# Optimization experiments

Hardware: AMD Instinct MI355X
Metric: run time of the kernel (lower is better)

Reference implementation:

```python
import jax, jax.numpy as jnp
import numpy as np
import math

T, B, N, D = 4, 4, 1024, 512
H = 8
HD = D // H
EPS = 1e-6


def setup_inputs() -> dict:
    key = jax.random.key(0)
    ks = jax.random.split(key, 9)
    s = 1.0 / math.sqrt(D)
    inp = {"x": jax.random.normal(ks[0], (T, B, N, D), dtype=jnp.float32)}
    names = ["wq", "wk", "wv", "wo"]
    for i, nm in enumerate(names):
        inp[nm] = jax.random.uniform(ks[1 + i], (D, D), dtype=jnp.float32, minval=-s, maxval=s)
        inp["b" + nm[1]] = jax.random.uniform(ks[5 + i], (D,), dtype=jnp.float32, minval=-s, maxval=s)
    return inp


def reference(x, wq, bq, wk, bk, wv, bv, wo, bo):
    t, b, n, d = x.shape
    # torch Linear: y = x @ W.T + bias
    q = x @ wq.T + bq
    k = x @ wk.T + bk
    v = x @ wv.T + bv
    # (t, b, n, H, HD) -> (t, b, H, n, HD)
    qh = q.reshape(t, b, n, H, HD).transpose(0, 1, 3, 2, 4)
    kh = k.reshape(t, b, n, H, HD).transpose(0, 1, 3, 2, 4)
    vh = v.reshape(t, b, n, H, HD).transpose(0, 1, 3, 2, 4)
    scores = jnp.einsum("tbhqd,tbhkd->tbhqk", qh, kh) / math.sqrt(HD)
    attn = jax.nn.relu(scores)
    attn = attn / (attn.sum(axis=-1, keepdims=True) + EPS)
    ctx = jnp.einsum("tbhqk,tbhkd->tbhqd", attn, vh)
    out = ctx.transpose(0, 1, 3, 2, 4).reshape(t, b, n, d)
    return out @ wo.T + bo
```

## Files before the change

### kernel.cpp

```cpp
#include <hip/hip_runtime.h>

typedef unsigned short u16;
typedef __attribute__((ext_vector_type(8))) short bf16x8;
typedef __attribute__((ext_vector_type(4))) float f32x4;
typedef __attribute__((ext_vector_type(16))) float f32x16;
typedef __attribute__((ext_vector_type(2))) unsigned int u32x2;

__device__ inline u16 f2b(float f) {
    unsigned u;
    __builtin_memcpy(&u, &f, 4);
    unsigned r = u + 0x7FFF + ((u >> 16) & 1);
    return (u16)(r >> 16);
}

__device__ inline bf16x8 pack8(const float* p) {
    union { u16 us[8]; bf16x8 v; } r;
#pragma unroll
    for (int i = 0; i < 8; i++) r.us[i] = f2b(p[i]);
    return r.v;
}

__device__ inline unsigned cvtpk(float lo, float hi) {
    unsigned r;
    asm("v_cvt_pk_bf16_f32 %0, %1, %2" : "=v"(r) : "v"(lo), "v"(hi));
    return r;
}

__device__ inline void gload16(const void* g, void* l) {
    __builtin_amdgcn_global_load_lds((__attribute__((address_space(1))) void*)g,
                                     (__attribute__((address_space(3))) void*)l, 16, 0, 0);
}

__global__ __launch_bounds__(256) void conv_kernel(const float* __restrict__ x,
                                                   const float* __restrict__ wq,
                                                   const float* __restrict__ wk,
                                                   const float* __restrict__ wv,
                                                   const float* __restrict__ wo,
                                                   u16* __restrict__ xb, u16* __restrict__ wb) {
    const int bid = blockIdx.x;
    const float* src;
    u16* dst;
    size_t base;
    if (bid < 4096) {
        src = x; dst = xb; base = (size_t)bid * 2048;
    } else {
        const int wsel = (bid - 4096) >> 7;
        src = (wsel == 0) ? wq : (wsel == 1) ? wk : (wsel == 2) ? wv : wo;
        dst = wb + (size_t)wsel * 262144;
        base = (size_t)((bid - 4096) & 127) * 2048;
    }
    const size_t idx = base + (size_t)threadIdx.x * 8;
    float a[8];
    *(float4*)&a[0] = *(const float4*)&src[idx];
    *(float4*)&a[4] = *(const float4*)&src[idx + 4];
    *(bf16x8*)&dst[idx] = pack8(a);
}

template <int MODE>
__global__ __launch_bounds__(256) void gemm_kernel(const u16* __restrict__ A,
                                                   const u16* __restrict__ W,
                                                   const float* __restrict__ B0,
                                                   const float* __restrict__ B1,
                                                   const float* __restrict__ B2,
                                                   void* __restrict__ O0v, u16* __restrict__ O1,
                                                   u16* __restrict__ O2) {
    const int m0 = blockIdx.x * 128;
    const int n0 = blockIdx.y * 128;
    const int seg = (MODE == 0) ? (n0 >> 9) : 0;
    const int nl0 = (MODE == 0) ? (n0 & 511) : n0;
    const float* Bb = (seg == 0) ? B0 : (seg == 1) ? B1 : B2;
    u16* O = (seg == 0) ? (u16*)O0v : (seg == 1) ? O1 : O2;

    __shared__ __align__(16) u16 Al[128 * 32];
    __shared__ __align__(16) u16 Bl[128 * 32];

    const int tid = threadIdx.x;
    const int lane = tid & 63, wave = tid >> 6;
    const int quad = lane >> 4, col = lane & 15;
    const int wm = wave >> 1, wn = wave & 1;

    f32x4 acc[4][4];
#pragma unroll
    for (int i = 0; i < 4; i++)
#pragma unroll
        for (int j = 0; j < 4; j++) acc[i][j] = (f32x4){0.f, 0.f, 0.f, 0.f};

    for (int k0 = 0; k0 < 512; k0 += 32) {
#pragma unroll
        for (int sh = 0; sh < 4; sh++) {
            const int c = tid + sh * 256;
            const int cl = c & 511;
            const int row = cl >> 2, cc = (cl & 3) * 8;
            if (c < 512)
                gload16(&A[(size_t)(m0 + row) * 512 + k0 + cc], &Al[cl * 8]);
            else
                gload16(&W[(size_t)(n0 + row) * 512 + k0 + cc], &Bl[cl * 8]);
        }
        __syncthreads();
        bf16x8 af[4], bfr[4];
#pragma unroll
        for (int t = 0; t < 4; t++) {
            af[t] = *(const bf16x8*)&Al[(wm * 64 + t * 16 + col) * 32 + quad * 8];
            bfr[t] = *(const bf16x8*)&Bl[(wn * 64 + t * 16 + col) * 32 + quad * 8];
        }
#pragma unroll
        for (int i = 0; i < 4; i++)
#pragma unroll
            for (int j = 0; j < 4; j++)
                acc[i][j] = __builtin_amdgcn_mfma_f32_16x16x32_bf16(af[i], bfr[j], acc[i][j], 0, 0, 0);
        __syncthreads();
    }

    float bias[4];
#pragma unroll
    for (int j = 0; j < 4; j++) bias[j] = Bb[nl0 + wn * 64 + j * 16 + col];

#pragma unroll
    for (int i = 0; i < 4; i++) {
        const int mbase = m0 + wm * 64 + i * 16 + quad * 4;
#pragma unroll
        for (int j = 0; j < 4; j++) {
            const int nl = nl0 + wn * 64 + j * 16 + col;
            if (MODE == 1) {
                float* Of = (float*)O0v;
#pragma unroll
                for (int r = 0; r < 4; r++)
                    Of[(size_t)(mbase + r) * 512 + nl] = acc[i][j][r] + bias[j];
            } else {
                const int h = nl >> 6, hd = nl & 63;
                if (seg < 2) {
                    const float qs = (seg == 0) ? 0.125f : 1.f;
#pragma unroll
                    for (int r = 0; r < 4; r++) {
                        int m = mbase + r;
                        int s = m >> 10, tok = m & 1023;
                        O[(size_t)((s * 8 + h) * 1024 + tok) * 64 + hd] =
                            f2b((acc[i][j][r] + bias[j]) * qs);
                    }
                } else {
                    int s = mbase >> 10, tok0 = mbase & 1023;
                    union { u16 us[4]; uint2 v; } pk;
#pragma unroll
                    for (int r = 0; r < 4; r++) pk.us[r] = f2b(acc[i][j][r] + bias[j]);
                    *(uint2*)&O[(size_t)((s * 8 + h) * 64 + hd) * 1024 + tok0] = pk.v;
                }
            }
        }
    }
}

__global__ __launch_bounds__(256) void attn_kernel(const u16* __restrict__ Q,
                                                   const u16* __restrict__ Kp,
                                                   const u16* __restrict__ Vt,
                                                   u16* __restrict__ Ctx) {
    __shared__ __align__(16) u16 Kl[2][4096];
    __shared__ __align__(16) u16 Vl[2][4096];

    const int bid = blockIdx.x;
    const int head = bid & 127;
    const int qt = bid >> 7;
    const int s = head >> 3, h = head & 7;
    const u16* Qh = Q + (size_t)head * 65536;
    const u16* Kh = Kp + (size_t)head * 65536;
    const u16* Vh = Vt + (size_t)head * 65536;

    const int tid = threadIdx.x;
    const int lane = tid & 63, wave = tid >> 6;
    const int l31 = lane & 31, hi = lane >> 5;
    const int q0 = qt * 128 + wave * 32;
    const int cx = l31 & 7;

    int srow[2], sxc[2];
#pragma unroll
    for (int i = 0; i < 2; i++) {
        const int p = tid + i * 256;
        srow[i] = p >> 3;
        sxc[i] = (p & 7) ^ (srow[i] & 7);
    }

#define STAGE(B, K0)                                                                  \
    {                                                                                 \
        _Pragma("unroll") for (int i_ = 0; i_ < 2; i_++) {                            \
            const int p_ = tid + i_ * 256;                                            \
            gload16(&Kh[(size_t)((K0) + srow[i_]) * 64 + sxc[i_] * 8], &Kl[B][p_ * 8]); \
        }                                                                             \
        _Pragma("unroll") for (int i_ = 0; i_ < 2; i_++) {                            \
            const int p_ = tid + i_ * 256;                                            \
            gload16(&Vh[(size_t)srow[i_] * 1024 + (K0) + sxc[i_] * 8], &Vl[B][p_ * 8]); \
        }                                                                             \
    }

    union { u16 us[8]; bf16x8 v; } one;
#pragma unroll
    for (int i = 0; i < 8; i++) one.us[i] = 0x3F80;
    const bf16x8 onesf = one.v;

    bf16x8 qf[4];
#pragma unroll
    for (int kk = 0; kk < 4; kk++)
        qf[kk] = *(const bf16x8*)&Qh[(size_t)(q0 + l31) * 64 + kk * 16 + hi * 8];

    f32x16 cacc[2], dacc;
#pragma unroll
    for (int r = 0; r < 16; r++) { cacc[0][r] = 0.f; cacc[1][r] = 0.f; dacc[r] = 0.f; }

    STAGE(0, 0)
    __syncthreads();

    int buf = 0;
    for (int kt = 0; kt < 16; kt++) {
        if (kt < 15) STAGE(buf ^ 1, (kt + 1) * 64)

        bf16x8 pa[4];
#pragma unroll
        for (int mt = 0; mt < 2; mt++) {
            f32x16 sacc;
#pragma unroll
            for (int r = 0; r < 16; r++) sacc[r] = 0.f;
            __builtin_amdgcn_s_setprio(1);
#pragma unroll
            for (int kk = 0; kk < 4; kk++) {
                const bf16x8 kf =
                    *(const bf16x8*)&Kl[buf][((mt * 32 + l31) * 8 + ((2 * kk + hi) ^ cx)) * 8];
                sacc = __builtin_amdgcn_mfma_f32_32x32x16_bf16(kf, qf[kk], sacc, 0, 0, 0);
            }
            __builtin_amdgcn_s_setprio(0);

            const unsigned c0 = cvtpk(fmaxf(sacc[0], 0.f), fmaxf(sacc[1], 0.f));
            const unsigned c1 = cvtpk(fmaxf(sacc[2], 0.f), fmaxf(sacc[3], 0.f));
            const unsigned c2 = cvtpk(fmaxf(sacc[4], 0.f), fmaxf(sacc[5], 0.f));
            const unsigned c3 = cvtpk(fmaxf(sacc[6], 0.f), fmaxf(sacc[7], 0.f));
            const unsigned c4 = cvtpk(fmaxf(sacc[8], 0.f), fmaxf(sacc[9], 0.f));
            const unsigned c5 = cvtpk(fmaxf(sacc[10], 0.f), fmaxf(sacc[11], 0.f));
            const unsigned c6 = cvtpk(fmaxf(sacc[12], 0.f), fmaxf(sacc[13], 0.f));
            const unsigned c7 = cvtpk(fmaxf(sacc[14], 0.f), fmaxf(sacc[15], 0.f));
            const u32x2 s02 = __builtin_amdgcn_permlane32_swap(c0, c2, false, false);
            const u32x2 s13 = __builtin_amdgcn_permlane32_swap(c1, c3, false, false);
            const u32x2 s46 = __builtin_amdgcn_permlane32_swap(c4, c6, false, false);
            const u32x2 s57 = __builtin_amdgcn_permlane32_swap(c5, c7, false, false);
            union { unsigned u[4]; bf16x8 v; } f0, f1;
            f0.u[0] = s02.x; f0.u[1] = s13.x; f0.u[2] = s02.y; f0.u[3] = s13.y;
            f1.u[0] = s46.x; f1.u[1] = s57.x; f1.u[2] = s46.y; f1.u[3] = s57.y;
            pa[mt * 2 + 0] = f0.v;
            pa[mt * 2 + 1] = f1.v;
        }

        __builtin_amdgcn_s_setprio(1);
#pragma unroll
        for (int kg = 0; kg < 4; kg++) {
            const bf16x8 vf0 = *(const bf16x8*)&Vl[buf][(l31 * 8 + ((2 * kg + hi) ^ cx)) * 8];
            const bf16x8 vf1 =
                *(const bf16x8*)&Vl[buf][(((32 + l31)) * 8 + ((2 * kg + hi) ^ cx)) * 8];
            dacc = __builtin_amdgcn_mfma_f32_32x32x16_bf16(pa[kg], onesf, dacc, 0, 0, 0);
            cacc[0] = __builtin_amdgcn_mfma_f32_32x32x16_bf16(pa[kg], vf0, cacc[0], 0, 0, 0);
            cacc[1] = __builtin_amdgcn_mfma_f32_32x32x16_bf16(pa[kg], vf1, cacc[1], 0, 0, 0);
        }
        __builtin_amdgcn_s_setprio(0);

        __syncthreads();
        buf ^= 1;
    }
#undef STAGE

#pragma unroll
    for (int r = 0; r < 16; r++) {
        const int ql = (r & 3) + 8 * (r >> 2) + 4 * hi;
        const float inv = 1.f / (dacc[r] + 1e-6f);
        const size_t grow = (size_t)(s * 1024 + q0 + ql);
        Ctx[grow * 512 + h * 64 + l31] = f2b(cacc[0][r] * inv);
        Ctx[grow * 512 + h * 64 + 32 + l31] = f2b(cacc[1][r] * inv);
    }
}

extern "C" void kernel_launch(void* const* d_in, const int* in_sizes, int n_in, void* d_out,
                              int out_size, void* d_ws, size_t ws_size, hipStream_t stream) {
    const float* x = (const float*)d_in[0];
    const float* wq = (const float*)d_in[1];
    const float* bq = (const float*)d_in[2];
    const float* wk = (const float*)d_in[3];
    const float* bk = (const float*)d_in[4];
    const float* wv = (const float*)d_in[5];
    const float* bv = (const float*)d_in[6];
    const float* wo = (const float*)d_in[7];
    const float* bo = (const float*)d_in[8];

    const size_t E = 16384ull * 512ull;
    u16* xb = (u16*)d_ws;
    u16* cw = xb;
    u16* wb = xb + E;
    u16* qw = wb + 4 * 262144;
    u16* kw = qw + E;
    u16* vw = kw + E;

    conv_kernel<<<dim3(4096 + 512), 256, 0, stream>>>(x, wq, wk, wv, wo, xb, wb);
    gemm_kernel<0><<<dim3(128, 12), 256, 0, stream>>>(xb, wb, bq, bk, bv, qw, kw, vw);
    attn_kernel<<<dim3(1024), 256, 0, stream>>>(qw, kw, vw, cw);
    gemm_kernel<1><<<dim3(128, 4), 256, 0, stream>>>(cw, wb + 3 * 262144, bo, nullptr, nullptr,
                                                     d_out, nullptr, nullptr);
}
```

Measured before the change: 206.7 us.

## Double attention query tile per wave to reuse staged K/V fragments

Each wave now handles 64 query rows instead of 32, so a block covers 256 queries and the grid is halved to 512 blocks. Every K and V fragment read from shared memory feeds two MFMA chains, which halves K/V global staging and LDS reads per query. A launch-bounds hint of 2 blocks per CU is added. The cost is twice the accumulator registers per wave, which may lower occupancy, and fewer blocks to spread across the CUs.

```diff
diff --git a/kernel.cpp b/kernel.cpp
--- a/kernel.cpp
+++ b/kernel.cpp
@@ -149,10 +149,10 @@
     }
 }
 
-__global__ __launch_bounds__(256) void attn_kernel(const u16* __restrict__ Q,
-                                                   const u16* __restrict__ Kp,
-                                                   const u16* __restrict__ Vt,
-                                                   u16* __restrict__ Ctx) {
+__global__ __launch_bounds__(256, 2) void attn_kernel(const u16* __restrict__ Q,
+                                                      const u16* __restrict__ Kp,
+                                                      const u16* __restrict__ Vt,
+                                                      u16* __restrict__ Ctx) {
     __shared__ __align__(16) u16 Kl[2][4096];
     __shared__ __align__(16) u16 Vl[2][4096];
 
@@ -167,7 +167,7 @@
     const int tid = threadIdx.x;
     const int lane = tid & 63, wave = tid >> 6;
     const int l31 = lane & 31, hi = lane >> 5;
-    const int q0 = qt * 128 + wave * 32;
+    const int q0 = qt * 256 + wave * 64;
     const int cx = l31 & 7;
 
     int srow[2], sxc[2];
@@ -178,16 +178,16 @@
         sxc[i] = (p & 7) ^ (srow[i] & 7);
     }
 
-#define STAGE(B, K0)                                                                  \
-    {                                                                                 \
-        _Pragma("unroll") for (int i_ = 0; i_ < 2; i_++) {                            \
-            const int p_ = tid + i_ * 256;                                            \
+#define STAGE(B, K0)                                                                    \
+    {                                                                                   \
+        _Pragma("unroll") for (int i_ = 0; i_ < 2; i_++) {                              \
+            const int p_ = tid + i_ * 256;                                              \
             gload16(&Kh[(size_t)((K0) + srow[i_]) * 64 + sxc[i_] * 8], &Kl[B][p_ * 8]); \
-        }                                                                             \
-        _Pragma("unroll") for (int i_ = 0; i_ < 2; i_++) {                            \
-            const int p_ = tid + i_ * 256;                                            \
+        }                                                                               \
+        _Pragma("unroll") for (int i_ = 0; i_ < 2; i_++) {                              \
+            const int p_ = tid + i_ * 256;                                              \
             gload16(&Vh[(size_t)srow[i_] * 1024 + (K0) + sxc[i_] * 8], &Vl[B][p_ * 8]); \
-        }                                                                             \
+        }                                                                               \
     }
 
     union { u16 us[8]; bf16x8 v; } one;
@@ -195,14 +195,25 @@
     for (int i = 0; i < 8; i++) one.us[i] = 0x3F80;
     const bf16x8 onesf = one.v;
 
-    bf16x8 qf[4];
-#pragma unroll
-    for (int kk = 0; kk < 4; kk++)
-        qf[kk] = *(const bf16x8*)&Qh[(size_t)(q0 + l31) * 64 + kk * 16 + hi * 8];
-
-    f32x16 cacc[2], dacc;
-#pragma unroll
-    for (int r = 0; r < 16; r++) { cacc[0][r] = 0.f; cacc[1][r] = 0.f; dacc[r] = 0.f; }
+    bf16x8 qf[2][4];
+#pragma unroll
+    for (int q2 = 0; q2 < 2; q2++)
+#pragma unroll
+        for (int kk = 0; kk < 4; kk++)
+            qf[q2][kk] =
+                *(const bf16x8*)&Qh[(size_t)(q0 + q2 * 32 + l31) * 64 + kk * 16 + hi * 8];
+
+    f32x16 cacc[2][2];
+    f32x16 dacc[2];
+#pragma unroll
+    for (int q2 = 0; q2 < 2; q2++) {
+#pragma unroll
+        for (int r = 0; r < 16; r++) {
+            cacc[q2][0][r] = 0.f;
+            cacc[q2][1][r] = 0.f;
+            dacc[q2][r] = 0.f;
+        }
+    }
 
     STAGE(0, 0)
     __syncthreads();
@@ -211,38 +222,43 @@
     for (int kt = 0; kt < 16; kt++) {
         if (kt < 15) STAGE(buf ^ 1, (kt + 1) * 64)
 
-        bf16x8 pa[4];
+        bf16x8 pa[2][4];
 #pragma unroll
         for (int mt = 0; mt < 2; mt++) {
-            f32x16 sacc;
-#pragma unroll
-            for (int r = 0; r < 16; r++) sacc[r] = 0.f;
+            f32x16 s0, s1;
+#pragma unroll
+            for (int r = 0; r < 16; r++) { s0[r] = 0.f; s1[r] = 0.f; }
             __builtin_amdgcn_s_setprio(1);
 #pragma unroll
             for (int kk = 0; kk < 4; kk++) {
                 const bf16x8 kf =
                     *(const bf16x8*)&Kl[buf][((mt * 32 + l31) * 8 + ((2 * kk + hi) ^ cx)) * 8];
-                sacc = __builtin_amdgcn_mfma_f32_32x32x16_bf16(kf, qf[kk], sacc, 0, 0, 0);
+                s0 = __builtin_amdgcn_mfma_f32_32x32x16_bf16(kf, qf[0][kk], s0, 0, 0, 0);
+                s1 = __builtin_amdgcn_mfma_f32_32x32x16_bf16(kf, qf[1][kk], s1, 0, 0, 0);
             }
             __builtin_amdgcn_s_setprio(0);
 
-            const unsigned c0 = cvtpk(fmaxf(sacc[0], 0.f), fmaxf(sacc[1], 0.f));
-            const unsigned c1 = cvtpk(fmaxf(sacc[2], 0.f), fmaxf(sacc[3], 0.f));
-            const unsigned c2 = cvtpk(fmaxf(sacc[4], 0.f), fmaxf(sacc[5], 0.f));
-            const unsigned c3 = cvtpk(fmaxf(sacc[6], 0.f), fmaxf(sacc[7], 0.f));
-            const unsigned c4 = cvtpk(fmaxf(sacc[8], 0.f), fmaxf(sacc[9], 0.f));
-            const unsigned c5 = cvtpk(fmaxf(sacc[10], 0.f), fmaxf(sacc[11], 0.f));
-            const unsigned c6 = cvtpk(fmaxf(sacc[12], 0.f), fmaxf(sacc[13], 0.f));
-            const unsigned c7 = cvtpk(fmaxf(sacc[14], 0.f), fmaxf(sacc[15], 0.f));
-            const u32x2 s02 = __builtin_amdgcn_permlane32_swap(c0, c2, false, false);
-            const u32x2 s13 = __builtin_amdgcn_permlane32_swap(c1, c3, false, false);
-            const u32x2 s46 = __builtin_amdgcn_permlane32_swap(c4, c6, false, false);
-            const u32x2 s57 = __builtin_amdgcn_permlane32_swap(c5, c7, false, false);
-            union { unsigned u[4]; bf16x8 v; } f0, f1;
-            f0.u[0] = s02.x; f0.u[1] = s13.x; f0.u[2] = s02.y; f0.u[3] = s13.y;
-            f1.u[0] = s46.x; f1.u[1] = s57.x; f1.u[2] = s46.y; f1.u[3] = s57.y;
-            pa[mt * 2 + 0] = f0.v;
-            pa[mt * 2 + 1] = f1.v;
+#pragma unroll
+            for (int q2 = 0; q2 < 2; q2++) {
+                const f32x16& sc = q2 ? s1 : s0;
+                const unsigned c0 = cvtpk(fmaxf(sc[0], 0.f), fmaxf(sc[1], 0.f));
+                const unsigned c1 = cvtpk(fmaxf(sc[2], 0.f), fmaxf(sc[3], 0.f));
+                const unsigned c2 = cvtpk(fmaxf(sc[4], 0.f), fmaxf(sc[5], 0.f));
+                const unsigned c3 = cvtpk(fmaxf(sc[6], 0.f), fmaxf(sc[7], 0.f));
+                const unsigned c4 = cvtpk(fmaxf(sc[8], 0.f), fmaxf(sc[9], 0.f));
+                const unsigned c5 = cvtpk(fmaxf(sc[10], 0.f), fmaxf(sc[11], 0.f));
+                const unsigned c6 = cvtpk(fmaxf(sc[12], 0.f), fmaxf(sc[13], 0.f));
+                const unsigned c7 = cvtpk(fmaxf(sc[14], 0.f), fmaxf(sc[15], 0.f));
+                const u32x2 s02 = __builtin_amdgcn_permlane32_swap(c0, c2, false, false);
+                const u32x2 s13 = __builtin_amdgcn_permlane32_swap(c1, c3, false, false);
+                const u32x2 s46 = __builtin_amdgcn_permlane32_swap(c4, c6, false, false);
+                const u32x2 s57 = __builtin_amdgcn_permlane32_swap(c5, c7, false, false);
+                union { unsigned u[4]; bf16x8 v; } f0u, f1u;
+                f0u.u[0] = s02.x; f0u.u[1] = s13.x; f0u.u[2] = s02.y; f0u.u[3] = s13.y;
+                f1u.u[0] = s46.x; f1u.u[1] = s57.x; f1u.u[2] = s46.y; f1u.u[3] = s57.y;
+                pa[q2][mt * 2 + 0] = f0u.v;
+                pa[q2][mt * 2 + 1] = f1u.v;
+            }
         }
 
         __builtin_amdgcn_s_setprio(1);
@@ -250,10 +266,13 @@
         for (int kg = 0; kg < 4; kg++) {
             const bf16x8 vf0 = *(const bf16x8*)&Vl[buf][(l31 * 8 + ((2 * kg + hi) ^ cx)) * 8];
             const bf16x8 vf1 =
-                *(const bf16x8*)&Vl[buf][(((32 + l31)) * 8 + ((2 * kg + hi) ^ cx)) * 8];
-            dacc = __builtin_amdgcn_mfma_f32_32x32x16_bf16(pa[kg], onesf, dacc, 0, 0, 0);
-            cacc[0] = __builtin_amdgcn_mfma_f32_32x32x16_bf16(pa[kg], vf0, cacc[0], 0, 0, 0);
-            cacc[1] = __builtin_amdgcn_mfma_f32_32x32x16_bf16(pa[kg], vf1, cacc[1], 0, 0, 0);
+                *(const bf16x8*)&Vl[buf][((32 + l31) * 8 + ((2 * kg + hi) ^ cx)) * 8];
+            dacc[0] = __builtin_amdgcn_mfma_f32_32x32x16_bf16(pa[0][kg], onesf, dacc[0], 0, 0, 0);
+            dacc[1] = __builtin_amdgcn_mfma_f32_32x32x16_bf16(pa[1][kg], onesf, dacc[1], 0, 0, 0);
+            cacc[0][0] = __builtin_amdgcn_mfma_f32_32x32x16_bf16(pa[0][kg], vf0, cacc[0][0], 0, 0, 0);
+            cacc[0][1] = __builtin_amdgcn_mfma_f32_32x32x16_bf16(pa[0][kg], vf1, cacc[0][1], 0, 0, 0);
+            cacc[1][0] = __builtin_amdgcn_mfma_f32_32x32x16_bf16(pa[1][kg], vf0, cacc[1][0], 0, 0, 0);
+            cacc[1][1] = __builtin_amdgcn_mfma_f32_32x32x16_bf16(pa[1][kg], vf1, cacc[1][1], 0, 0, 0);
         }
         __builtin_amdgcn_s_setprio(0);
 
@@ -263,12 +282,15 @@
 #undef STAGE
 
 #pragma unroll
-    for (int r = 0; r < 16; r++) {
-        const int ql = (r & 3) + 8 * (r >> 2) + 4 * hi;
-        const float inv = 1.f / (dacc[r] + 1e-6f);
-        const size_t grow = (size_t)(s * 1024 + q0 + ql);
-        Ctx[grow * 512 + h * 64 + l31] = f2b(cacc[0][r] * inv);
-        Ctx[grow * 512 + h * 64 + 32 + l31] = f2b(cacc[1][r] * inv);
+    for (int q2 = 0; q2 < 2; q2++) {
+#pragma unroll
+        for (int r = 0; r < 16; r++) {
+            const int ql = (r & 3) + 8 * (r >> 2) + 4 * hi;
+            const float inv = 1.f / (dacc[q2][r] + 1e-6f);
+            const size_t grow = (size_t)(s * 1024 + q0 + q2 * 32 + ql);
+            Ctx[grow * 512 + h * 64 + l31] = f2b(cacc[q2][0][r] * inv);
+            Ctx[grow * 512 + h * 64 + 32 + l31] = f2b(cacc[q2][1][r] * inv);
+        }
     }
 }
 
@@ -294,7 +316,7 @@
 
     conv_kernel<<<dim3(4096 + 512), 256, 0, stream>>>(x, wq, wk, wv, wo, xb, wb);
     gemm_kernel<0><<<dim3(128, 12), 256, 0, stream>>>(xb, wb, bq, bk, bv, qw, kw, vw);
-    attn_kernel<<<dim3(1024), 256, 0, stream>>>(qw, kw, vw, cw);
+    attn_kernel<<<dim3(512), 256, 0, stream>>>(qw, kw, vw, cw);
     gemm_kernel<1><<<dim3(128, 4), 256, 0, stream>>>(cw, wb + 3 * 262144, bo, nullptr, nullptr,
                                                      d_out, nullptr, nullptr);
 }
```

Result: faster. 197.7 us (-4.4%).
